# Optimization experiments

Hardware: AMD Instinct MI355X
Metric: run time of the kernel (lower is better)

Reference implementation:

```python
import math
import jax, jax.numpy as jnp
import numpy as np

WS = 4            # window size
LS = 2 * WS       # local context size
NH = 8            # num heads
DIM = 128
EPS = 1e-5


def setup_inputs() -> dict:
    key = jax.random.key(0)
    ks = jax.random.split(key, 8)
    B, C, H, W = 4, DIM, 48, 48
    features = jax.random.normal(ks[0], (B, C, H, W), dtype=jnp.float32)
    s = 0.02
    return {
        'features': features,
        'ln_w': jnp.ones((C,), jnp.float32),
        'ln_b': jnp.zeros((C,), jnp.float32),
        'q_w': jax.random.normal(ks[1], (C, C), jnp.float32) * s,
        'q_b': jnp.zeros((C,), jnp.float32),
        'kv_w': jax.random.normal(ks[2], (2 * C, C), jnp.float32) * s,
        'kv_b': jnp.zeros((2 * C,), jnp.float32),
        'out_w': jax.random.normal(ks[3], (C, C), jnp.float32) * s,
        'out_b': jnp.zeros((C,), jnp.float32),
    }


def _avgpool_tokens(x, k):
    # x: [B,C,H,W] -> [B, (H//k)*(W//k), C]
    B, C, H, W = x.shape
    t = x.reshape(B, C, H // k, k, W // k, k).mean(axis=(3, 5))
    return t.reshape(B, C, -1).transpose(0, 2, 1)


def reference(features, ln_w, ln_b, q_w, q_b, kv_w, kv_b, out_w, out_b):
    B, C, H, W = features.shape
    Hw, Ww = H // WS, W // WS
    nw = Hw * Ww
    hd = C // NH

    # ---- window partition: [B,C,H,W] -> [B*nw, WS*WS, C]
    qt = features.reshape(B, C, Hw, WS, Ww, WS).transpose(0, 2, 4, 3, 5, 1)
    qt = qt.reshape(B * nw, WS * WS, C)

    # ---- LayerNorm(dim)
    mu = qt.mean(-1, keepdims=True)
    var = qt.var(-1, keepdims=True)
    qt = (qt - mu) / jnp.sqrt(var + EPS) * ln_w + ln_b

    # ---- local context: pad to target, unfold kernel=LS stride=WS
    target = (int(math.sqrt(nw)) - 1) * WS + LS
    ph, pw = max(0, target - H), max(0, target - W)
    pad = ((0, 0), (0, 0), (ph // 2, ph - ph // 2), (pw // 2, pw - pw // 2))
    padded = jnp.pad(features, pad)
    # channel order of patches is (C, kh, kw), same as torch unfold
    patches = jax.lax.conv_general_dilated_patches(
        padded, filter_shape=(LS, LS), window_strides=(WS, WS), padding='VALID')
    local = patches.reshape(B, C, LS * LS, nw).transpose(0, 3, 2, 1)
    local = local.reshape(B * nw, LS * LS, C)

    # ---- multi-scale pooled tokens, broadcast to each window
    mid = _avgpool_tokens(features, 2)      # [B, M, C]
    glo = _avgpool_tokens(features, 4)      # [B, G, C]
    mid = jnp.broadcast_to(mid[:, None], (B, nw) + mid.shape[1:]).reshape(B * nw, -1, C)
    glo = jnp.broadcast_to(glo[:, None], (B, nw) + glo.shape[1:]).reshape(B * nw, -1, C)

    kv_tokens = jnp.concatenate([local, mid, glo], axis=1)  # [B*nw, Nkv, C]

    # ---- projections (torch Linear: x @ W.T + b)
    queries = qt @ q_w.T + q_b
    kv = kv_tokens @ kv_w.T + kv_b
    keys, values = kv[..., :C], kv[..., C:]

    # ---- multi-head attention
    Nq, Nkv = queries.shape[1], keys.shape[1]
    q = queries.reshape(-1, Nq, NH, hd)
    k = keys.reshape(-1, Nkv, NH, hd)
    v = values.reshape(-1, Nkv, NH, hd)
    scores = jnp.einsum('bqhd,bkhd->bhqk', q, k) / math.sqrt(hd)
    weights = jax.nn.softmax(scores, axis=-1)
    attended = jnp.einsum('bhqk,bkhd->bqhd', weights, v).reshape(-1, Nq, C)

    out = attended @ out_w.T + out_b

    # ---- window reconstruction -> [B,C,H,W]
    out = out.reshape(B, Hw, Ww, WS, WS, C).transpose(0, 5, 1, 3, 2, 4)
    out = out.reshape(B, C, H, W)
    return out + features
```

## Files before the change

### kernel.cpp

```cpp
#include <hip/hip_runtime.h>


typedef unsigned short u16;
typedef short v8s __attribute__((ext_vector_type(8)));
typedef v8s __attribute__((may_alias)) v8s_am;
typedef short v4s __attribute__((ext_vector_type(4)));
typedef v4s __attribute__((may_alias)) v4s_am;
typedef float v4f __attribute__((ext_vector_type(4)));

#define MFMA_BF16(a, b, c) __builtin_amdgcn_mfma_f32_16x16x32_bf16(a, b, c, 0, 0, 0)

#if __has_builtin(__builtin_amdgcn_mfma_f32_16x16x16bf16_1k)
#define MFMA16(a, b, c) __builtin_amdgcn_mfma_f32_16x16x16bf16_1k(a, b, c, 0, 0, 0)
#else
static __device__ __forceinline__ v4f mfma16_fb(v4s a, v4s b, v4f c) {
    v8s a8 = {a[0], a[1], a[2], a[3], 0, 0, 0, 0};
    v8s b8 = {b[0], b[1], b[2], b[3], 0, 0, 0, 0};
    return MFMA_BF16(a8, b8, c);
}
#define MFMA16(a, b, c) mfma16_fb(a, b, c)
#endif

#if __has_builtin(__builtin_amdgcn_exp2f)
#define EXP2(x) __builtin_amdgcn_exp2f(x)
#else
#define EXP2(x) exp2f(x)
#endif

__device__ __forceinline__ float b2f(u16 u) {
    union { unsigned int i; float f; } x;
    x.i = ((unsigned int)u) << 16;
    return x.f;
}
__device__ __forceinline__ u16 f2b(float f) {
    union { float f; unsigned int i; } x;
    x.f = f;
    unsigned int u = x.i;
    return (u16)((u + 0x7fffu + ((u >> 16) & 1u)) >> 16);
}

__global__ __launch_bounds__(256) void k_prep(
    const float* __restrict__ F,
    const float* __restrict__ qw, const float* __restrict__ kvw,
    const float* __restrict__ ow,
    const float* __restrict__ lnw, const float* __restrict__ lnb,
    const float* __restrict__ kvb,
    u16* __restrict__ Xt, u16* __restrict__ Wb, float* __restrict__ MuRs,
    u16* __restrict__ Pml, u16* __restrict__ Vlh)
{
    int blk = blockIdx.x;
    int t = threadIdx.x;
    if (blk >= 484) {
        int base = (blk - 484) * 8192 + t * 32;
#pragma unroll
        for (int k = 0; k < 4; ++k) {
            int off = base + k * 8;
            int ch = off / 10816;
            u16 bv = f2b(kvb[128 + ch]);
            v8s o = {(short)bv, (short)bv, (short)bv, (short)bv,
                     (short)bv, (short)bv, (short)bv, (short)bv};
            *(v8s_am*)&Vlh[off] = o;
        }
        return;
    }
    if (blk >= 304) {
        int gid = (blk - 304) * 256 + t;
        int row = gid >> 4;
        int seg = gid & 15;
        v8s outv;
        if (row < 2304) {
            int b = row / 576, r = row % 576;
            int i = r / 24, j = r % 24;
#pragma unroll
            for (int jc = 0; jc < 8; ++jc) {
                int c = seg * 8 + jc;
                const float* src = F + ((size_t)(b * 128 + c)) * 2304 + (2 * i) * 48 + 2 * j;
                float2 a = *(const float2*)src;
                float2 d = *(const float2*)(src + 48);
                outv[jc] = (short)f2b((a.x + a.y + d.x + d.y) * 0.25f);
            }
        } else {
            int r2 = row - 2304;
            int b = r2 / 144, r = r2 % 144;
            int i = r / 12, j = r % 12;
#pragma unroll
            for (int jc = 0; jc < 8; ++jc) {
                int c = seg * 8 + jc;
                const float* src = F + ((size_t)(b * 128 + c)) * 2304 + (4 * i) * 48 + 4 * j;
                float s = 0.f;
#pragma unroll
                for (int di = 0; di < 4; ++di) {
                    float4 v = *(const float4*)(src + di * 48);
                    s += (v.x + v.y) + (v.z + v.w);
                }
                outv[jc] = (short)f2b(s * 0.0625f);
            }
        }
        *(v8s_am*)&Pml[((size_t)row) * 128 + seg * 8] = outv;
        return;
    }
    if (blk >= 288) {
        int base = (blk - 288) * 4096 + t * 16;
#pragma unroll
        for (int i = 0; i < 4; ++i) {
            int idx = base + i * 4;
            const float* src; int off;
            if (idx < 16384)      { src = qw;  off = idx; }
            else if (idx < 49152) { src = kvw; off = idx - 16384; }
            else                  { src = ow;  off = idx - 49152; }
            float4 v = *(const float4*)(src + off);
            unsigned long long packed =
                (unsigned long long)f2b(v.x) |
                ((unsigned long long)f2b(v.y) << 16) |
                ((unsigned long long)f2b(v.z) << 32) |
                ((unsigned long long)f2b(v.w) << 48);
            *(unsigned long long*)(Wb + idx) = packed;
        }
        if (blk == 288) {
            Wb[65536 + t] = f2b(t < 128 ? lnw[t] : lnb[t - 128]);
            Wb[65792 + t] = f2b(kvb[t]);
        }
        return;
    }
    __shared__ u16 X[128][34];
    int b = blk / 72;
    int p0 = (blk % 72) * 32;
#pragma unroll 4
    for (int i = 0; i < 16; ++i) {
        int c = i * 8 + (t >> 5);
        int pix = t & 31;
        X[c][pix] = f2b(F[((size_t)(b * 128 + c)) * 2304 + p0 + pix]);
    }
    __syncthreads();
    int pix = t >> 3;
    int c0 = (t & 7) * 16;
    size_t row = (size_t)(b * 2304 + p0 + pix) * 128;
    float s = 0.f, s2 = 0.f;
#pragma unroll
    for (int sg = 0; sg < 2; ++sg) {
        v8s raw;
#pragma unroll
        for (int j = 0; j < 8; ++j) {
            u16 u = X[c0 + sg * 8 + j][pix];
            raw[j] = (short)u;
            float v = b2f(u);
            s += v; s2 += v * v;
        }
        *(v8s_am*)&Xt[row + c0 + sg * 8] = raw;
    }
    s += __shfl_xor(s, 1);  s2 += __shfl_xor(s2, 1);
    s += __shfl_xor(s, 2);  s2 += __shfl_xor(s2, 2);
    s += __shfl_xor(s, 4);  s2 += __shfl_xor(s2, 4);
    if ((t & 7) == 0) {
        float mean = s * (1.f / 128.f);
        float var = s2 * (1.f / 128.f) - mean * mean;
        float rstd = rsqrtf(var + 1e-5f);
        MuRs[(b * 2304 + p0 + pix) * 2]     = mean;
        MuRs[(b * 2304 + p0 + pix) * 2 + 1] = rstd;
    }
}

__global__ __launch_bounds__(256) void k_gemm_kv(
    const u16* __restrict__ Xt,
    const u16* __restrict__ Pml,
    const u16* __restrict__ W,
    const float* __restrict__ bias,
    u16* __restrict__ KVh,
    u16* __restrict__ VTg,
    u16* __restrict__ Klh,
    u16* __restrict__ Vlh)
{
    __shared__ u16 Al[64][136];
    __shared__ u16 Wl[64][136];
    int gb = blockIdx.x;
    bool loc = (gb < 144);
    int tm = loc ? gb * 64 : (gb - 144) * 64;
    int tn = blockIdx.y * 64;
    int t = threadIdx.x;
    {
        int seg = t & 15, r0 = t >> 4;
        const u16* A = loc ? Xt : Pml;
#pragma unroll
        for (int i = 0; i < 4; ++i) {
            int r = r0 + 16 * i;
            *(v8s_am*)&Al[r][seg * 8] = *(const v8s_am*)&A[((size_t)(tm + r)) * 128 + seg * 8];
            *(v8s_am*)&Wl[r][seg * 8] = *(const v8s_am*)&W[((size_t)(tn + r)) * 128 + seg * 8];
        }
    }
    __syncthreads();
    int lane = t & 63, wave = t >> 6;
    int n15 = lane & 15, quad = lane >> 4;
    int wm = (wave & 1) * 32, wn = (wave >> 1) * 32;
    v4f acc[2][2] = {};
#pragma unroll
    for (int kc = 0; kc < 4; ++kc) {
        v8s a[2], bb[2];
#pragma unroll
        for (int im = 0; im < 2; ++im)
            a[im] = *(const v8s_am*)&Al[wm + im * 16 + n15][kc * 32 + quad * 8];
#pragma unroll
        for (int in = 0; in < 2; ++in)
            bb[in] = *(const v8s_am*)&Wl[wn + in * 16 + n15][kc * 32 + quad * 8];
#pragma unroll
        for (int im = 0; im < 2; ++im)
#pragma unroll
            for (int in = 0; in < 2; ++in)
                acc[im][in] = MFMA_BF16(a[im], bb[in], acc[im][in]);
    }
#pragma unroll
    for (int in = 0; in < 2; ++in) {
        int n = tn + wn + in * 16 + n15;
        float bv = bias[n];
#pragma unroll
        for (int im = 0; im < 2; ++im) {
            int mbase = tm + wm + im * 16 + quad * 4;
#pragma unroll
            for (int r = 0; r < 4; ++r) {
                int m = mbase + r;
                u16 h = f2b(acc[im][in][r] + bv);
                if (loc) {
                    int b = m / 2304, px = m % 2304;
                    if (n < 128) {
                        Klh[(((size_t)(n >> 4) * 4 + b) * 2304 + px) * 16 + (n & 15)] = h;
                    } else {
                        int ch = n - 128;
                        int hh = px / 48, ww = px % 48;
                        Vlh[((size_t)(ch * 4 + b)) * 2704 + (hh + 2) * 52 + ww + 2] = h;
                    }
                } else {
                    if (n < 128) {
                        KVh[((size_t)(n >> 4) * 2880 + m) * 16 + (n & 15)] = h;
                    } else {
                        int ch = n - 128, bb2, tok;
                        if (m < 2304) { bb2 = m / 576; tok = m % 576; }
                        else { int r2 = m - 2304; bb2 = r2 / 144; tok = 576 + r2 % 144; }
                        VTg[((size_t)(bb2 * 128 + ch)) * 720 + tok] = h;
                    }
                }
            }
        }
    }
}

__global__ __launch_bounds__(512, 3) void k_attn_fused(
    const float* __restrict__ F,
    const u16* __restrict__ Xt,
    const float* __restrict__ MuRs,
    const u16* __restrict__ KVh,
    const u16* __restrict__ VTg,
    const u16* __restrict__ Klh,
    const u16* __restrict__ Vlh,
    const u16* __restrict__ Wb,
    const float* __restrict__ qb,
    const float* __restrict__ ob,
    float* __restrict__ Out)
{
    __shared__ u16 KP[8][64][16];
    __shared__ u16 At[16][136];

    const u16* qwb  = Wb;
    const u16* owb  = Wb + 49152;
    const u16* lnwb = Wb + 65536;
    const u16* lnbb = Wb + 65664;
    const u16* kvbb = Wb + 65792;

    int blk = blockIdx.x;
    int xcd = blk & 7, jj = blk >> 3;
    int b = xcd >> 1;
    int wr = (xcd & 1) * 6 + jj / 12;
    int wc = jj % 12;

    int t = threadIdx.x;
    int lane = t & 63, wave = t >> 6, n15 = lane & 15, quad = lane >> 4;
    v4f zz4 = {0.f, 0.f, 0.f, 0.f};
    const float QSCALE = 0.25f * 1.44269504f;

    u16* KPw = &KP[wave][0][0];
    const u16* kwave = KVh + (size_t)wave * 46080;
    const u16* vrow0 = VTg + (size_t)b * 92160
                     + (size_t)(wave * 16 + n15) * 720 + quad * 4;

    int fh = lane >> 3, fw = lane & 7;
    int hh = wr * 4 - 2 + fh, ww = wc * 4 - 2 + fw;
    bool kvalid = (hh >= 0 && hh < 48 && ww >= 0 && ww < 48);
    int hc = min(max(hh, 0), 47), wcc = min(max(ww, 0), 47);
    v8s kN0, kN1;
    {
        const u16* s = Klh + ((size_t)((wave * 4 + b) * 2304 + hc * 48 + wcc)) * 16;
        kN0 = *(const v8s_am*)s; kN1 = *(const v8s_am*)(s + 8);
    }

    int qh = wr * 4 + (n15 >> 2), qw_ = wc * 4 + (n15 & 3);
    int qpix = b * 2304 + qh * 48 + qw_;
    float mu = MuRs[qpix * 2], rstd = MuRs[qpix * 2 + 1];
    v8s xln[4];
#pragma unroll
    for (int kc = 0; kc < 4; ++kc) {
        v8s x  = *(const v8s_am*)&Xt[(size_t)qpix * 128 + kc * 32 + quad * 8];
        v8s lw = *(const v8s_am*)&lnwb[kc * 32 + quad * 8];
        v8s lb = *(const v8s_am*)&lnbb[kc * 32 + quad * 8];
        v8s y;
#pragma unroll
        for (int j = 0; j < 8; ++j)
            y[j] = (short)f2b((b2f((u16)x[j]) - mu) * rstd * b2f((u16)lw[j]) + b2f((u16)lb[j]));
        xln[kc] = y;
    }

    v4s qf;
    {
        int n0 = wave * 16;
        v4f qacc = zz4;
#pragma unroll
        for (int kc = 0; kc < 4; ++kc) {
            v8s aw = *(const v8s_am*)&qwb[((size_t)(n0 + n15)) * 128 + kc * 32 + quad * 8];
            qacc = MFMA_BF16(aw, xln[kc], qacc);
        }
#pragma unroll
        for (int r = 0; r < 4; ++r)
            qf[r] = (short)f2b((qacc[r] + qb[n0 + quad * 4 + r]) * QSCALE);
    }

    {
        v8s kb0 = *(const v8s_am*)&kvbb[wave * 16];
        v8s kb1 = *(const v8s_am*)&kvbb[wave * 16 + 8];
        if (!kvalid) { kN0 = kb0; kN1 = kb1; }
    }

    v4f oacc = zz4;
    float ls = 0.f;

    *(v8s_am*)&KPw[lane * 16]     = kN0;
    *(v8s_am*)&KPw[lane * 16 + 8] = kN1;
    {
        const u16* s = kwave + (size_t)(b * 576 + lane) * 16;
        kN0 = *(const v8s_am*)s; kN1 = *(const v8s_am*)(s + 8);
    }

    {
        const u16* vbaseL = Vlh + ((size_t)((wave * 16 + n15) * 4 + b)) * 2704
                          + (wr * 4 + (quad >> 1)) * 52 + wc * 4 + (quad & 1) * 4;
#pragma unroll
        for (int g = 0; g < 4; ++g) {
            v4s kf = *(const v4s_am*)&KPw[(g * 16 + n15) * 16 + quad * 4];
            v4s vf = *(const v4s_am*)(vbaseL + g * 104);
            v4f St = MFMA16(kf, qf, zz4);
            float p0 = EXP2(St[0]), p1 = EXP2(St[1]);
            float p2 = EXP2(St[2]), p3 = EXP2(St[3]);
            ls += (p0 + p1) + (p2 + p3);
            v4s pk = {(short)f2b(p0), (short)f2b(p1), (short)f2b(p2), (short)f2b(p3)};
            oacc = MFMA16(vf, pk, oacc);
        }
    }

    *(v8s_am*)&KPw[lane * 16]     = kN0;
    *(v8s_am*)&KPw[lane * 16 + 8] = kN1;
    {
        const u16* s = kwave + (size_t)(b * 576 + 64 + lane) * 16;
        kN0 = *(const v8s_am*)s; kN1 = *(const v8s_am*)(s + 8);
    }

    for (int tb = 0; tb <= 10; ++tb) {
        v4s kf[4];
#pragma unroll
        for (int g = 0; g < 4; ++g)
            kf[g] = *(const v4s_am*)&KPw[(g * 16 + n15) * 16 + quad * 4];
        *(v8s_am*)&KPw[lane * 16]     = kN0;
        *(v8s_am*)&KPw[lane * 16 + 8] = kN1;
        if (tb < 10) {
            int t2 = tb + 2;
            int row = (t2 < 9) ? (b * 576 + t2 * 64 + lane)
                               : (2304 + b * 144 + (t2 - 9) * 64 + lane);
            if (t2 == 11) row = 2304 + b * 144 + 128 + n15;
            const u16* s = kwave + (size_t)row * 16;
            kN0 = *(const v8s_am*)s; kN1 = *(const v8s_am*)(s + 8);
        }
        v4s vp[4];
#pragma unroll
        for (int g = 0; g < 4; ++g)
            vp[g] = *(const v4s_am*)(vrow0 + tb * 64 + g * 16);
#pragma unroll
        for (int g = 0; g < 4; ++g) {
            v4f St = MFMA16(kf[g], qf, zz4);
            float p0 = EXP2(St[0]), p1 = EXP2(St[1]);
            float p2 = EXP2(St[2]), p3 = EXP2(St[3]);
            ls += (p0 + p1) + (p2 + p3);
            v4s pk = {(short)f2b(p0), (short)f2b(p1), (short)f2b(p2), (short)f2b(p3)};
            oacc = MFMA16(vp[g], pk, oacc);
        }
    }
    {
        v4s kf = *(const v4s_am*)&KPw[n15 * 16 + quad * 4];
        v4s vf = *(const v4s_am*)(vrow0 + 704);
        v4f St = MFMA16(kf, qf, zz4);
        float p0 = EXP2(St[0]), p1 = EXP2(St[1]);
        float p2 = EXP2(St[2]), p3 = EXP2(St[3]);
        ls += (p0 + p1) + (p2 + p3);
        v4s pk = {(short)f2b(p0), (short)f2b(p1), (short)f2b(p2), (short)f2b(p3)};
        oacc = MFMA16(vf, pk, oacc);
    }

    ls += __shfl_xor(ls, 16);
    ls += __shfl_xor(ls, 32);
    {
        float inv = 1.f / ls;
        v4s a4 = {(short)f2b(oacc[0] * inv), (short)f2b(oacc[1] * inv),
                  (short)f2b(oacc[2] * inv), (short)f2b(oacc[3] * inv)};
        *(v4s_am*)&At[n15][wave * 16 + quad * 4] = a4;
    }
    __syncthreads();

    {
        int n0 = wave * 16;
        v4f oa = zz4;
#pragma unroll
        for (int kc = 0; kc < 4; ++kc) {
            v8s af = *(const v8s_am*)&At[n15][kc * 32 + quad * 8];
            v8s bf = *(const v8s_am*)&owb[((size_t)(n0 + n15)) * 128 + kc * 32 + quad * 8];
            oa = MFMA_BF16(af, bf, oa);
        }
        int c = n0 + n15;
        float bv = ob[c];
#pragma unroll
        for (int r = 0; r < 4; ++r) {
            int pix = quad * 4 + r;
            int hh2 = wr * 4 + (pix >> 2), ww2 = wc * 4 + (pix & 3);
            size_t idx = ((size_t)(b * 128 + c)) * 2304 + hh2 * 48 + ww2;
            Out[idx] = oa[r] + bv + F[idx];
        }
    }
}

extern "C" void kernel_launch(void* const* d_in, const int* in_sizes, int n_in,
                              void* d_out, int out_size, void* d_ws, size_t ws_size,
                              hipStream_t stream)
{
    const float* F   = (const float*)d_in[0];
    const float* lnw = (const float*)d_in[1];
    const float* lnb = (const float*)d_in[2];
    const float* qw  = (const float*)d_in[3];
    const float* qb  = (const float*)d_in[4];
    const float* kvw = (const float*)d_in[5];
    const float* kvb = (const float*)d_in[6];
    const float* ow  = (const float*)d_in[7];
    const float* ob  = (const float*)d_in[8];
    float* Out = (float*)d_out;

    u16* ws    = (u16*)d_ws;
    u16* Xt    = ws;
    u16* Pml   = Xt + 9216 * 128;
    u16* KVh   = Pml + 2880 * 128;
    u16* VTg   = KVh + 8 * 2880 * 16;
    u16* Klh   = VTg + 4 * 128 * 720;
    u16* Vlh   = Klh + 8 * 4 * 2304 * 16;
    u16* Wb    = Vlh + 128 * 4 * 2704;
    float* MuRs = (float*)(Wb + 66048);
    u16* kvwb = Wb + 16384;

    k_prep<<<653, 256, 0, stream>>>(F, qw, kvw, ow, lnw, lnb, kvb,
                                    Xt, Wb, MuRs, Pml, Vlh);
    k_gemm_kv<<<dim3(189, 4), 256, 0, stream>>>(Xt, Pml, kvwb, kvb,
                                                KVh, VTg, Klh, Vlh);
    k_attn_fused<<<576, 512, 0, stream>>>(F, Xt, MuRs, KVh, VTg, Klh, Vlh,
                                          Wb, qb, ob, Out);
}
```

Measured before the change: 121.6 us.

## Precompute LayerNorm output in prep and stage KV GEMM epilogue through LDS

The prep kernel now writes a normalized bf16 copy of the tokens (Xln), so the attention kernel just loads the LayerNorm result instead of recomputing it from Xt plus per-pixel mean/rstd. Separately, the KV GEMM epilogue first writes its tile into shared memory, transposing it for the V half, and then emits 16-byte vectorized global stores instead of scattered 2-byte stores. This cuts redundant LN math and uncoalesced writes, at the cost of an extra workspace buffer, more global writes in prep, and two extra barriers in the GEMM.

```diff
diff --git a/kernel.cpp b/kernel.cpp
--- a/kernel.cpp
+++ b/kernel.cpp
@@ -45,7 +45,7 @@
     const float* __restrict__ ow,
     const float* __restrict__ lnw, const float* __restrict__ lnb,
     const float* __restrict__ kvb,
-    u16* __restrict__ Xt, u16* __restrict__ Wb, float* __restrict__ MuRs,
+    u16* __restrict__ Xt, u16* __restrict__ Xln, u16* __restrict__ Wb,
     u16* __restrict__ Pml, u16* __restrict__ Vlh)
 {
     int blk = blockIdx.x;
@@ -123,6 +123,9 @@
         return;
     }
     __shared__ u16 X[128][34];
+    __shared__ float Lw[128], Lb[128];
+    if (t < 128) Lw[t] = lnw[t];
+    else         Lb[t - 128] = lnb[t - 128];
     int b = blk / 72;
     int p0 = (blk % 72) * 32;
 #pragma unroll 4
@@ -151,12 +154,19 @@
     s += __shfl_xor(s, 1);  s2 += __shfl_xor(s2, 1);
     s += __shfl_xor(s, 2);  s2 += __shfl_xor(s2, 2);
     s += __shfl_xor(s, 4);  s2 += __shfl_xor(s2, 4);
-    if ((t & 7) == 0) {
-        float mean = s * (1.f / 128.f);
-        float var = s2 * (1.f / 128.f) - mean * mean;
-        float rstd = rsqrtf(var + 1e-5f);
-        MuRs[(b * 2304 + p0 + pix) * 2]     = mean;
-        MuRs[(b * 2304 + p0 + pix) * 2 + 1] = rstd;
+    float mean = s * (1.f / 128.f);
+    float var = s2 * (1.f / 128.f) - mean * mean;
+    float rstd = rsqrtf(var + 1e-5f);
+#pragma unroll
+    for (int sg = 0; sg < 2; ++sg) {
+        v8s o;
+#pragma unroll
+        for (int j = 0; j < 8; ++j) {
+            int c = c0 + sg * 8 + j;
+            float v = b2f(X[c][pix]);
+            o[j] = (short)f2b((v - mean) * rstd * Lw[c] + Lb[c]);
+        }
+        *(v8s_am*)&Xln[row + c0 + sg * 8] = o;
     }
 }
 
@@ -207,36 +217,61 @@
             for (int in = 0; in < 2; ++in)
                 acc[im][in] = MFMA_BF16(a[im], bb[in], acc[im][in]);
     }
+    bool vdst = (tn >= 128);
+    __syncthreads();
+    u16* Ct = &Al[0][0];
 #pragma unroll
     for (int in = 0; in < 2; ++in) {
-        int n = tn + wn + in * 16 + n15;
-        float bv = bias[n];
+        int nl = wn + in * 16 + n15;
+        float bv = bias[tn + nl];
 #pragma unroll
         for (int im = 0; im < 2; ++im) {
-            int mbase = tm + wm + im * 16 + quad * 4;
 #pragma unroll
             for (int r = 0; r < 4; ++r) {
-                int m = mbase + r;
+                int ml = wm + im * 16 + quad * 4 + r;
                 u16 h = f2b(acc[im][in][r] + bv);
-                if (loc) {
-                    int b = m / 2304, px = m % 2304;
-                    if (n < 128) {
-                        Klh[(((size_t)(n >> 4) * 4 + b) * 2304 + px) * 16 + (n & 15)] = h;
-                    } else {
-                        int ch = n - 128;
-                        int hh = px / 48, ww = px % 48;
-                        Vlh[((size_t)(ch * 4 + b)) * 2704 + (hh + 2) * 52 + ww + 2] = h;
-                    }
-                } else {
-                    if (n < 128) {
-                        KVh[((size_t)(n >> 4) * 2880 + m) * 16 + (n & 15)] = h;
-                    } else {
-                        int ch = n - 128, bb2, tok;
-                        if (m < 2304) { bb2 = m / 576; tok = m % 576; }
-                        else { int r2 = m - 2304; bb2 = r2 / 144; tok = 576 + r2 % 144; }
-                        VTg[((size_t)(bb2 * 128 + ch)) * 720 + tok] = h;
-                    }
+                Ct[vdst ? (nl * 72 + ml) : (ml * 72 + nl)] = h;
+            }
+        }
+    }
+    __syncthreads();
+    {
+        int a = t >> 2, sub = t & 3;
+        v8s a0 = *(const v8s_am*)&Ct[a * 72 + sub * 16];
+        v8s a1 = *(const v8s_am*)&Ct[a * 72 + sub * 16 + 8];
+        if (!vdst) {
+            int m = tm + a;
+            int headc = (tn >> 4) + sub;
+            size_t d; u16* dst;
+            if (loc) { int b = m / 2304, px = m % 2304;
+                       d = (((size_t)(headc * 4 + b)) * 2304 + px) * 16; dst = Klh; }
+            else     { d = ((size_t)headc * 2880 + m) * 16; dst = KVh; }
+            *(v8s_am*)&dst[d]     = a0;
+            *(v8s_am*)&dst[d + 8] = a1;
+        } else {
+            int ch = (tn - 128) + a;
+            int pxo = sub * 16;
+            if (loc) {
+                int b = tm / 2304;
+                int s2_ = tm % 2304 + pxo;
+                int hh = s2_ / 48, ww = s2_ % 48;
+                size_t base = ((size_t)(ch * 4 + b)) * 2704 + (hh + 2) * 52 + ww + 2;
+                union { v8s s; unsigned int u[4]; } u0, u1;
+                u0.s = a0; u1.s = a1;
+#pragma unroll
+                for (int k = 0; k < 4; ++k) {
+                    *(unsigned int*)&Vlh[base + 2 * k]     = u0.u[k];
+                    *(unsigned int*)&Vlh[base + 8 + 2 * k] = u1.u[k];
                 }
+            } else {
+                int m = tm + pxo;
+                size_t base;
+                if (m < 2304) { int b = m / 576, tok = m % 576;
+                                base = ((size_t)(b * 128 + ch)) * 720 + tok; }
+                else { int r2 = m - 2304; int b = r2 / 144, tok = 576 + r2 % 144;
+                       base = ((size_t)(b * 128 + ch)) * 720 + tok; }
+                *(v8s_am*)&VTg[base]     = a0;
+                *(v8s_am*)&VTg[base + 8] = a1;
             }
         }
     }
@@ -244,8 +279,7 @@
 
 __global__ __launch_bounds__(512, 3) void k_attn_fused(
     const float* __restrict__ F,
-    const u16* __restrict__ Xt,
-    const float* __restrict__ MuRs,
+    const u16* __restrict__ Xln,
     const u16* __restrict__ KVh,
     const u16* __restrict__ VTg,
     const u16* __restrict__ Klh,
@@ -260,8 +294,6 @@
 
     const u16* qwb  = Wb;
     const u16* owb  = Wb + 49152;
-    const u16* lnwb = Wb + 65536;
-    const u16* lnbb = Wb + 65664;
     const u16* kvbb = Wb + 65792;
 
     int blk = blockIdx.x;
@@ -292,19 +324,10 @@
 
     int qh = wr * 4 + (n15 >> 2), qw_ = wc * 4 + (n15 & 3);
     int qpix = b * 2304 + qh * 48 + qw_;
-    float mu = MuRs[qpix * 2], rstd = MuRs[qpix * 2 + 1];
     v8s xln[4];
 #pragma unroll
-    for (int kc = 0; kc < 4; ++kc) {
-        v8s x  = *(const v8s_am*)&Xt[(size_t)qpix * 128 + kc * 32 + quad * 8];
-        v8s lw = *(const v8s_am*)&lnwb[kc * 32 + quad * 8];
-        v8s lb = *(const v8s_am*)&lnbb[kc * 32 + quad * 8];
-        v8s y;
-#pragma unroll
-        for (int j = 0; j < 8; ++j)
-            y[j] = (short)f2b((b2f((u16)x[j]) - mu) * rstd * b2f((u16)lw[j]) + b2f((u16)lb[j]));
-        xln[kc] = y;
-    }
+    for (int kc = 0; kc < 4; ++kc)
+        xln[kc] = *(const v8s_am*)&Xln[(size_t)qpix * 128 + kc * 32 + quad * 8];
 
     v4s qf;
     {
@@ -447,19 +470,19 @@
 
     u16* ws    = (u16*)d_ws;
     u16* Xt    = ws;
-    u16* Pml   = Xt + 9216 * 128;
+    u16* Xln   = Xt + 9216 * 128;
+    u16* Pml   = Xln + 9216 * 128;
     u16* KVh   = Pml + 2880 * 128;
     u16* VTg   = KVh + 8 * 2880 * 16;
     u16* Klh   = VTg + 4 * 128 * 720;
     u16* Vlh   = Klh + 8 * 4 * 2304 * 16;
     u16* Wb    = Vlh + 128 * 4 * 2704;
-    float* MuRs = (float*)(Wb + 66048);
     u16* kvwb = Wb + 16384;
 
     k_prep<<<653, 256, 0, stream>>>(F, qw, kvw, ow, lnw, lnb, kvb,
-                                    Xt, Wb, MuRs, Pml, Vlh);
+                                    Xt, Xln, Wb, Pml, Vlh);
     k_gemm_kv<<<dim3(189, 4), 256, 0, stream>>>(Xt, Pml, kvwb, kvb,
                                                 KVh, VTg, Klh, Vlh);
-    k_attn_fused<<<576, 512, 0, stream>>>(F, Xt, MuRs, KVh, VTg, Klh, Vlh,
+    k_attn_fused<<<576, 512, 0, stream>>>(F, Xln, KVh, VTg, Klh, Vlh,
                                           Wb, qb, ob, Out);
 }
```

After: 118.3 us. -2.7%, faster.
